# Performance work log

Hardware: AMD Instinct MI355X
Metric: run time of the kernel (lower is better)

Reference implementation:

```python
import jax, jax.numpy as jnp
import numpy as np

NUM_CLASSES = 80
STRIDES = (8, 16, 32)
RADIUS = 2.5
BOX_WEIGHT = 5.0
BIG = 1e9  # emulates restriction of cost/matching to union-candidate anchors
CAND_K = 10


def setup_inputs() -> dict:
    key = jax.random.key(0)
    ks = jax.random.split(key, 6)
    B, G = 16, 16
    p0 = jax.random.normal(ks[0], (B, NUM_CLASSES + 5, 160, 160), jnp.float32)
    p1 = jax.random.normal(ks[1], (B, NUM_CLASSES + 5, 80, 80), jnp.float32)
    p2 = jax.random.normal(ks[2], (B, NUM_CLASSES + 5, 40, 40), jnp.float32)
    cxy = jax.random.uniform(ks[3], (B, G, 2), jnp.float32, 64.0, 1216.0)
    wh = jax.random.uniform(ks[4], (B, G, 2), jnp.float32, 16.0, 256.0)
    cls = jax.random.randint(ks[5], (B, G, 1), 0, NUM_CLASSES).astype(jnp.float32)
    labels = jnp.concatenate([cxy, wh, cls], axis=-1)  # [B,G,5] xywh + class id
    return {"p0": p0, "p1": p1, "p2": p2, "labels": labels}


def _decode(p, stride):
    # [B,C,H,W] -> [B,HW,C] with xy=(xy+grid)*stride, wh=exp(wh)*stride
    B, C, H, W = p.shape
    out = jnp.transpose(p.reshape(B, C, H * W), (0, 2, 1))
    yy, xx = jnp.meshgrid(jnp.arange(H, dtype=p.dtype), jnp.arange(W, dtype=p.dtype), indexing='ij')
    gx, gy = xx.reshape(-1), yy.reshape(-1)
    xy = (out[..., :2] + jnp.stack([gx, gy], axis=-1)) * stride
    wh = jnp.exp(out[..., 2:4]) * stride
    return jnp.concatenate([xy, wh, out[..., 4:]], axis=-1), gx, gy


def _pair_iou(a, b):
    # a:[G,4], b:[A,4] in xywh -> [G,A]
    a1, a2 = a[:, :2] - a[:, 2:] * 0.5, a[:, :2] + a[:, 2:] * 0.5
    b1, b2 = b[:, :2] - b[:, 2:] * 0.5, b[:, :2] + b[:, 2:] * 0.5
    tl = jnp.maximum(a1[:, None], b1[None])
    br = jnp.minimum(a2[:, None], b2[None])
    wh = jnp.maximum(br - tl, 0.0)
    inter = wh[..., 0] * wh[..., 1]
    return inter / (a[:, 2] * a[:, 3])[:, None].__add__((b[:, 2] * b[:, 3])[None]).__sub__(inter).__add__(1e-16)


def _elem_iou(a, b):
    # elementwise xywh iou on [...,4]
    a1, a2 = a[..., :2] - a[..., 2:] * 0.5, a[..., :2] + a[..., 2:] * 0.5
    b1, b2 = b[..., :2] - b[..., 2:] * 0.5, b[..., :2] + b[..., 2:] * 0.5
    wh = jnp.maximum(jnp.minimum(a2, b2) - jnp.maximum(a1, b1), 0.0)
    inter = wh[..., 0] * wh[..., 1]
    return inter / (a[..., 2] * a[..., 3] + b[..., 2] * b[..., 3] - inter + 1e-16)


def _bce_logits(x, t):
    return jnp.maximum(x, 0.0) - x * t + jnp.log1p(jnp.exp(-jnp.abs(x)))


def _assign(tb, tc, pbox, pcls_l, pconf_l, xc, yc, sv):
    # Per-image SimOTA. tb:[G,4] tc:[G] pbox:[A,4] pcls_l:[A,C] pconf_l:[A]
    G = tb.shape[0]
    bx, by, bw, bh = tb[:, 0:1], tb[:, 1:2], tb[:, 2:3], tb[:, 3:4]
    in_box = (xc[None] > bx - bw * 0.5) & (xc[None] < bx + bw * 0.5) & \
             (yc[None] > by - bh * 0.5) & (yc[None] < by + bh * 0.5)  # [G,A]
    r = RADIUS * sv[None]
    in_mir = (xc[None] > bx - r) & (xc[None] < bx + r) & (yc[None] > by - r) & (yc[None] < by + r)
    union = jnp.any(in_box, 0) | jnp.any(in_mir, 0)  # [A]
    inter = in_box & in_mir  # [G,A]
    iou = _pair_iou(tb, pbox)  # [G,A]
    # cls cost: BCE(sqrt(sigmoid(cls)*sigmoid(conf)), one_hot) summed over classes
    p = jnp.sqrt(jax.nn.sigmoid(pcls_l) * jax.nn.sigmoid(pconf_l)[:, None])  # [A,C]
    logp = jnp.clip(jnp.log(p), -100.0, None)
    log1mp = jnp.clip(jnp.log1p(-p), -100.0, None)
    base = -log1mp.sum(-1)  # [A] = sum_c -log(1-p)
    cls_cost = base[None] - logp[:, tc].T + log1mp[:, tc].T  # [G,A]
    cost = cls_cost - 3.0 * jnp.log(iou + 1e-8) + 1e5 * (~inter) + BIG * (~union)[None]
    iou_m = jnp.where(union[None], iou, 0.0)
    dyn_k = jnp.maximum(jax.lax.top_k(iou_m, CAND_K)[0].sum(1).astype(jnp.int32), 1)  # [G]
    _, idx = jax.lax.top_k(-cost, CAND_K)  # per-gt lowest-cost anchors, sorted
    sel = (jnp.arange(CAND_K)[None] < dyn_k[:, None]).astype(cost.dtype)  # [G,K]
    matching = jnp.zeros_like(cost).at[jnp.arange(G)[:, None], idx].max(sel)  # [G,A]
    conflict = matching.sum(0) > 1.0
    gt_min = jnp.argmin(cost, axis=0)  # [A]
    onehot_min = (jnp.arange(G)[:, None] == gt_min[None]).astype(cost.dtype)
    matching = jnp.where(conflict[None], onehot_min, matching)
    fg = matching.sum(0) > 0.0  # [A]
    gidx = jnp.argmax(matching, axis=0)  # [A]
    miou = (matching * iou).sum(0)  # [A]
    t_cls = jax.nn.one_hot(tc[gidx], NUM_CLASSES, dtype=cost.dtype) * miou[:, None]  # [A,C]
    t_box = tb[gidx]  # [A,4]
    return fg, t_cls, t_box


def _forward(p0, p1, p2, labels):
    outs, xcs, ycs, svs = [], [], [], []
    for p, s in zip((p0, p1, p2), STRIDES):
        o, gx, gy = _decode(p, float(s))
        outs.append(o)
        xcs.append((gx + 0.5) * s)
        ycs.append((gy + 0.5) * s)
        svs.append(jnp.full_like(gx, s))
    out = jnp.concatenate(outs, axis=1)  # [B,A,85]
    xc, yc, sv = jnp.concatenate(xcs), jnp.concatenate(ycs), jnp.concatenate(svs)
    pbox, pconf, pcls = out[..., :4], out[..., 4], out[..., 5:]
    tb, tc = labels[..., :4], labels[..., 4].astype(jnp.int32)
    assign = jax.vmap(_assign, in_axes=(0, 0, 0, 0, 0, None, None, None))
    fg, t_cls, t_box = jax.lax.stop_gradient(assign(tb, tc, pbox, pcls, pconf, xc, yc, sv))
    fgf = fg.astype(pbox.dtype)  # target_conf == final fg mask
    loss_box = (fgf * (1.0 - _elem_iou(pbox, t_box) ** 2)).sum()
    loss_conf = _bce_logits(pconf, fgf).sum()
    loss_cls = (fgf[..., None] * _bce_logits(pcls, t_cls)).sum()
    fg_num = jnp.maximum(fgf.sum(), 1.0)
    return (BOX_WEIGHT * loss_box + loss_conf + loss_cls) / fg_num


def reference(p0, p1, p2, labels):
    return _forward(p0, p1, p2, labels)
```

## Files before the change

### kernel.cpp

```cpp
#include <hip/hip_runtime.h>
#include <hip/hip_bf16.h>
#include <cstdint>

#define NCLS 80
#define GNUM 16
#define BNUM 16
#define A0   25600
#define A1   6400
#define A2   1600
#define ATOT 33600
#define QTOT 16800
#define NBLK_A 132
#define NBLK_TOTAL (NBLK_A*BNUM)
#define NSPLIT 8
#define SEG   4200
#define WSEG  1050
#define NWAVE 32
#define FINF  3.4e38f
#define IINF  0x7fffffff

__device__ __forceinline__ float rcpf(float x){ return __builtin_amdgcn_rcpf(x); }
__device__ __forceinline__ float sqf (float x){ return __builtin_amdgcn_sqrtf(x); }
__device__ __forceinline__ float rsqf(float x){ return __builtin_amdgcn_rsqf(x); }

__device__ __forceinline__ float bce(float x, float t){
  float e = __expf(-fabsf(x));
  return fmaxf(x,0.f) - x*t + __logf(1.f + e);
}

__device__ __forceinline__ void get_level(const float* p0, const float* p1, const float* p2,
                                          int a, const float*& p, int& hw, int& off, int& W, float& s)
{
  if (a < A0){ p=p0; hw=A0; off=a; W=160; s=8.f; }
  else if (a < A0+A1){ p=p1; hw=A1; off=a-A0; W=80; s=16.f; }
  else { p=p2; hw=A2; off=a-A0-A1; W=40; s=32.f; }
}

__global__ __launch_bounds__(256, 4) void decode_cost_kernel(
    const float* __restrict__ p0, const float* __restrict__ p1, const float* __restrict__ p2,
    const float* __restrict__ labels,
    float* __restrict__ cost, float4* __restrict__ pbox, float* __restrict__ pconf,
    unsigned char* __restrict__ unionm)
{
  const int b = blockIdx.y;
  const int q = blockIdx.x*256 + threadIdx.x;
  __shared__ float s_tb[GNUM][4];
  __shared__ int   s_tc[GNUM];
  if (threadIdx.x < GNUM){
    const float* L = labels + ((size_t)b*GNUM + threadIdx.x)*5;
    s_tb[threadIdx.x][0]=L[0]; s_tb[threadIdx.x][1]=L[1];
    s_tb[threadIdx.x][2]=L[2]; s_tb[threadIdx.x][3]=L[3];
    s_tc[threadIdx.x]=(int)L[4];
  }
  __syncthreads();
  if (q >= QTOT) return;
  const int a0 = q*2;

  const float* p; int hw, off, W; float s;
  get_level(p0,p1,p2,a0,p,hw,off,W,s);
  const float* bp = p + (size_t)b*(NCLS+5)*hw + off;

  const float2 RX = *(const float2*)(bp);
  const float2 RY = *(const float2*)(bp + (size_t)hw);
  const float2 RW = *(const float2*)(bp + 2*(size_t)hw);
  const float2 RH = *(const float2*)(bp + 3*(size_t)hw);
  const float2 CL = *(const float2*)(bp + 4*(size_t)hw);
  const float* cp = bp + 5*(size_t)hw;

  int gx0 = off % W, gy0 = off / W;
  int gx1 = gx0+1, gy1 = gy0; if (gx1 >= W){ gx1 = 0; gy1++; }

  const float sc0 = rcpf(1.f + __expf(-CL.x));
  const float sc1 = rcpf(1.f + __expf(-CL.y));
  const float ssc0 = sqf(sc0),   ssc1 = sqf(sc1);
  const float rssc0 = rcpf(ssc0), rssc1 = rcpf(ssc1);

  float base0=0.f, base1=0.f;
  #pragma unroll 2
  for (int bt=0; bt<10; bt++){
    float2 xv[8];
    #pragma unroll
    for (int j=0;j<8;j++) xv[j] = *(const float2*)(cp + (size_t)(bt*8+j)*hw);
    float pr0=1.f, pr1=1.f;
    #pragma unroll
    for (int j=0;j<8;j++){
      pr0 *= (1.f - ssc0*rsqf(1.f+__expf(-xv[j].x)));
      pr1 *= (1.f - ssc1*rsqf(1.f+__expf(-xv[j].y)));
    }
    base0 -= __logf(pr0);
    base1 -= __logf(pr1);
  }

  const float px0=(RX.x+gx0)*s, py0=(RY.x+gy0)*s, pw0=__expf(RW.x)*s, ph0=__expf(RH.x)*s;
  const float px1=(RX.y+gx1)*s, py1=(RY.y+gy1)*s, pw1=__expf(RW.y)*s, ph1=__expf(RH.y)*s;
  const float xc0=(gx0+0.5f)*s, yc0=(gy0+0.5f)*s;
  const float xc1=(gx1+0.5f)*s, yc1=(gy1+0.5f)*s;
  const float q1x0=px0-pw0*0.5f, q2x0=px0+pw0*0.5f, q1y0=py0-ph0*0.5f, q2y0=py0+ph0*0.5f;
  const float q1x1=px1-pw1*0.5f, q2x1=px1+pw1*0.5f, q1y1=py1-ph1*0.5f, q2y1=py1+ph1*0.5f;
  const float areaP0 = pw0*ph0, areaP1 = pw1*ph1;
  const float r = 2.5f*s;

  bool un0=false, un1=false;
  #pragma unroll
  for (int g=0;g<GNUM;g++){
    const float bx=s_tb[g][0], by=s_tb[g][1], bw=s_tb[g][2], bh=s_tb[g][3];
    const float b1x=bx-bw*0.5f, b2x=bx+bw*0.5f, b1y=by-bh*0.5f, b2y=by+bh*0.5f;
    un0 = un0 || ((xc0>b1x)&&(xc0<b2x)&&(yc0>b1y)&&(yc0<b2y))
              || ((xc0>bx-r)&&(xc0<bx+r)&&(yc0>by-r)&&(yc0<by+r));
    un1 = un1 || ((xc1>b1x)&&(xc1<b2x)&&(yc1>b1y)&&(yc1<b2y))
              || ((xc1>bx-r)&&(xc1<bx+r)&&(yc1>by-r)&&(yc1<by+r));
  }
  const float add0 = un0?0.f:1e9f, add1 = un1?0.f:1e9f;

  const size_t rowb = (size_t)b*GNUM*ATOT + a0;

  #pragma unroll
  for (int g=0;g<GNUM;g++){
    const float2 x = *(const float2*)(cp + (size_t)s_tc[g]*hw);
    const float e0 = __expf(-x.x), e1 = __expf(-x.y);
    const float rp0 = rssc0*sqf(1.f+e0), rp1 = rssc1*sqf(1.f+e1);
    const float cd0 = __logf(fmaxf(rp0-1.f, 1e-30f));
    const float cd1 = __logf(fmaxf(rp1-1.f, 1e-30f));

    const float bx=s_tb[g][0], by=s_tb[g][1], bw=s_tb[g][2], bh=s_tb[g][3];
    const float b1x=bx-bw*0.5f, b2x=bx+bw*0.5f, b1y=by-bh*0.5f, b2y=by+bh*0.5f;
    const float areaB = bw*bh;

    const bool inb0 = (xc0>b1x)&&(xc0<b2x)&&(yc0>b1y)&&(yc0<b2y);
    const bool inm0 = (xc0>bx-r)&&(xc0<bx+r)&&(yc0>by-r)&&(yc0<by+r);
    const bool inb1 = (xc1>b1x)&&(xc1<b2x)&&(yc1>b1y)&&(yc1<b2y);
    const bool inm1 = (xc1>bx-r)&&(xc1<bx+r)&&(yc1>by-r)&&(yc1<by+r);

    float iw,ih,inte;
    iw = fmaxf(fminf(b2x,q2x0)-fmaxf(b1x,q1x0),0.f);
    ih = fmaxf(fminf(b2y,q2y0)-fmaxf(b1y,q1y0),0.f);
    inte = iw*ih;
    const float iou0 = inte * rcpf(areaB+areaP0-inte+1e-16f);
    iw = fmaxf(fminf(b2x,q2x1)-fmaxf(b1x,q1x1),0.f);
    ih = fmaxf(fminf(b2y,q2y1)-fmaxf(b1y,q1y1),0.f);
    inte = iw*ih;
    const float iou1 = inte * rcpf(areaB+areaP1-inte+1e-16f);

    float2 cst;
    cst.x = base0 + cd0 - 3.f*__logf(iou0+1e-8f) + ((inb0&&inm0)?0.f:100000.f) + add0;
    cst.y = base1 + cd1 - 3.f*__logf(iou1+1e-8f) + ((inb1&&inm1)?0.f:100000.f) + add1;
    *(float2*)(cost + rowb + (size_t)g*ATOT) = cst;
  }

  pbox[(size_t)b*ATOT+a0  ] = make_float4(px0,py0,pw0,ph0);
  pbox[(size_t)b*ATOT+a0+1] = make_float4(px1,py1,pw1,ph1);
  *(float2*)(pconf + (size_t)b*ATOT + a0) = make_float2(CL.x, CL.y);
  uchar2 um; um.x = un0?1:0; um.y = un1?1:0;
  *(uchar2*)(unionm + (size_t)b*ATOT + a0) = um;
}

__global__ __launch_bounds__(256) void topk_stage1(
    const float* __restrict__ cost, const float4* __restrict__ pbox,
    const unsigned char* __restrict__ unionm, const float* __restrict__ labels,
    float* __restrict__ cand_c, int* __restrict__ cand_i, float* __restrict__ cand_v)
{
  const int bg   = blockIdx.y;
  const int b    = bg >> 4;
  const int seg  = blockIdx.x;
  const int wave = threadIdx.x >> 6;
  const int lane = threadIdx.x & 63;
  const int wg   = seg*4 + wave;

  const float*  crow = cost + (size_t)bg*ATOT;
  const float4* prow = pbox + (size_t)b*ATOT;
  const unsigned char* urow = unionm + (size_t)b*ATOT;
  const float bx = labels[bg*5+0], by = labels[bg*5+1];
  const float bw = labels[bg*5+2], bh = labels[bg*5+3];
  const float areaB = bw*bh;
  const float b1x=bx-bw*0.5f, b2x=bx+bw*0.5f, b1y=by-bh*0.5f, b2y=by+bh*0.5f;

  const int start = seg*SEG + wave*WSEG;
  const int end   = start + WSEG;

  float cv[10]; int ci[10]; float iv[10];
  #pragma unroll
  for (int k=0;k<10;k++){ cv[k]=FINF; ci[k]=IINF; iv[k]=0.f; }

  for (int a = start + lane; a < end; a += 64){
    float c = crow[a];
    if (c < cv[9] || (c == cv[9] && a < ci[9])){
      float nc=c; int ni=a;
      #pragma unroll
      for (int k=0;k<10;k++){
        bool better = (nc < cv[k]) || (nc==cv[k] && ni<ci[k]);
        float tv=cv[k]; int ti=ci[k];
        cv[k]=better?nc:cv[k]; ci[k]=better?ni:ci[k];
        nc  =better?tv:nc;     ni  =better?ti:ni;
      }
    }
    if (urow[a]){
      float4 pb = prow[a];
      float tlx=fmaxf(b1x, pb.x-pb.z*0.5f), brx=fminf(b2x, pb.x+pb.z*0.5f);
      float tly=fmaxf(b1y, pb.y-pb.w*0.5f), bry=fminf(b2y, pb.y+pb.w*0.5f);
      float iw=fmaxf(brx-tlx,0.f), ih=fmaxf(bry-tly,0.f);
      float inte=iw*ih;
      float io = inte * rcpf(areaB + pb.z*pb.w - inte + 1e-16f);
      if (io > iv[9]){
        float nv=io;
        #pragma unroll
        for (int k=0;k<10;k++){
          bool better = nv > iv[k];
          float tv=iv[k];
          iv[k]=better?nv:iv[k];
          nv  =better?tv:nv;
        }
      }
    }
  }

  float selc = 0.f; int seli = 0;
  #pragma unroll
  for (int r=0;r<10;r++){
    float bv = cv[0]; int bi = ci[0];
    #pragma unroll
    for (int off=32; off>0; off>>=1){
      float ov = __shfl_xor(bv, off);
      int   oi = __shfl_xor(bi, off);
      bool take = (ov < bv) || (ov==bv && oi<bi);
      bv = take?ov:bv; bi = take?oi:bi;
    }
    if (lane == r){ selc = bv; seli = bi; }
    if (cv[0]==bv && ci[0]==bi){
      #pragma unroll
      for (int k=0;k<9;k++){ cv[k]=cv[k+1]; ci[k]=ci[k+1]; }
      cv[9]=FINF; ci[9]=IINF;
    }
  }
  float selv = 0.f;
  #pragma unroll
  for (int r=0;r<10;r++){
    float bv = iv[0]; int bl = lane;
    #pragma unroll
    for (int off=32; off>0; off>>=1){
      float ov = __shfl_xor(bv, off);
      int   ol = __shfl_xor(bl, off);
      bool take = (ov > bv) || (ov==bv && ol<bl);
      bv = take?ov:bv; bl = take?ol:bl;
    }
    if (lane == r) selv = bv;
    if (lane == bl){
      #pragma unroll
      for (int k=0;k<9;k++){ iv[k]=iv[k+1]; }
      iv[9]=0.f;
    }
  }

  if (lane < 10){
    const size_t base = ((size_t)bg*NWAVE + wg)*10 + lane;
    cand_c[base] = selc;
    cand_i[base] = seli;
    cand_v[base] = selv;
  }
}

__global__ __launch_bounds__(64) void topk_stage2(
    const float* __restrict__ cand_c, const int* __restrict__ cand_i,
    const float* __restrict__ cand_v, unsigned int* __restrict__ match_mask)
{
  const int bg = blockIdx.x;
  const int b = bg >> 4, g = bg & 15;
  const int lane = threadIdx.x;
  const size_t base = (size_t)bg*NWAVE*10 + lane*5;

  float cv[5]; int ci[5]; float iv[5];
  #pragma unroll
  for (int k=0;k<5;k++){ cv[k]=cand_c[base+k]; ci[k]=cand_i[base+k]; iv[k]=cand_v[base+k]; }

  int seli = 0;
  #pragma unroll
  for (int r=0;r<10;r++){
    float bv = cv[0]; int bi = ci[0];
    #pragma unroll
    for (int off=32; off>0; off>>=1){
      float ov = __shfl_xor(bv, off);
      int   oi = __shfl_xor(bi, off);
      bool take = (ov < bv) || (ov==bv && oi<bi);
      bv = take?ov:bv; bi = take?oi:bi;
    }
    if (lane == r) seli = bi;
    if (cv[0]==bv && ci[0]==bi){
      #pragma unroll
      for (int k=0;k<4;k++){ cv[k]=cv[k+1]; ci[k]=ci[k+1]; }
      cv[4]=FINF; ci[4]=IINF;
    }
  }

  float isum = 0.f;
  #pragma unroll
  for (int r=0;r<10;r++){
    float bv = iv[0]; int bl = lane;
    #pragma unroll
    for (int off=32; off>0; off>>=1){
      float ov = __shfl_xor(bv, off);
      int   ol = __shfl_xor(bl, off);
      bool take = (ov > bv) || (ov==bv && ol<bl);
      bv = take?ov:bv; bl = take?ol:bl;
    }
    isum += bv;
    if (lane == bl){
      #pragma unroll
      for (int k=0;k<4;k++){ iv[k]=iv[k+1]; }
      iv[4]=0.f;
    }
  }

  int dynk = (int)isum;
  if (dynk < 1)  dynk = 1;
  if (dynk > 10) dynk = 10;
  if (lane < dynk)
    atomicOr(&match_mask[(size_t)b*ATOT + seli], 1u<<g);
}

__global__ __launch_bounds__(256) void loss_kernel(
    const float* __restrict__ p0, const float* __restrict__ p1, const float* __restrict__ p2,
    const float* __restrict__ labels,
    const float* __restrict__ cost, const float4* __restrict__ pbox,
    const float* __restrict__ pconf, const unsigned int* __restrict__ match_mask,
    float* __restrict__ blocksums)
{
  const int b = blockIdx.y;
  const int a = blockIdx.x*256 + threadIdx.x;
  float lbox=0.f, lconf=0.f, lcls=0.f, fgn=0.f;
  if (a < ATOT){
    unsigned int m = match_mask[(size_t)b*ATOT+a];
    float cl = pconf[(size_t)b*ATOT+a];
    if (m != 0u){
      int gidx;
      if (__popc(m) > 1){
        float best = FINF; int bgi = 0;
        for (int g=0; g<GNUM; g++){
          float c = cost[((size_t)b*GNUM+g)*ATOT + a];
          if (c < best){ best=c; bgi=g; }
        }
        gidx = bgi;
      } else {
        gidx = __ffs(m)-1;
      }
      const float* L = labels + ((size_t)b*GNUM+gidx)*5;
      float bx=L[0], by=L[1], bw=L[2], bh=L[3];
      int tcg=(int)L[4];
      float4 pb = pbox[(size_t)b*ATOT+a];
      float tlx=fmaxf(bx-bw*0.5f, pb.x-pb.z*0.5f);
      float brx=fminf(bx+bw*0.5f, pb.x+pb.z*0.5f);
      float tly=fmaxf(by-bh*0.5f, pb.y-pb.w*0.5f);
      float bry=fminf(by+bh*0.5f, pb.y+pb.w*0.5f);
      float iw=fmaxf(brx-tlx,0.f), ih=fmaxf(bry-tly,0.f);
      float inte=iw*ih;
      float iou = inte * rcpf(bw*bh + pb.z*pb.w - inte + 1e-16f);
      lbox = 1.f - iou*iou;
      lconf = bce(cl, 1.f);
      float miou = iou;
      const float* p; int hw, off, W; float s;
      get_level(p0,p1,p2,a,p,hw,off,W,s);
      const float* bp = p + (size_t)b*(NCLS+5)*hw + off;
      for (int c=0;c<NCLS;c++){
        float x = bp[(size_t)(5+c)*hw];
        float t = (c==tcg)? miou : 0.f;
        lcls += bce(x, t);
      }
      fgn = 1.f;
    } else {
      lconf = bce(cl, 0.f);
    }
  }
  #pragma unroll
  for (int off2=32; off2>0; off2>>=1){
    lbox  += __shfl_down(lbox,  off2);
    lconf += __shfl_down(lconf, off2);
    lcls  += __shfl_down(lcls,  off2);
    fgn   += __shfl_down(fgn,   off2);
  }
  __shared__ float s_red[4][4];
  const int wave = threadIdx.x >> 6;
  if ((threadIdx.x & 63)==0){
    s_red[wave][0]=lbox; s_red[wave][1]=lconf; s_red[wave][2]=lcls; s_red[wave][3]=fgn;
  }
  __syncthreads();
  if (threadIdx.x==0){
    float r0=0,r1=0,r2=0,r3=0;
    #pragma unroll
    for (int w=0;w<4;w++){ r0+=s_red[w][0]; r1+=s_red[w][1]; r2+=s_red[w][2]; r3+=s_red[w][3]; }
    const int bid = blockIdx.y*gridDim.x + blockIdx.x;
    ((float4*)blocksums)[bid] = make_float4(r0,r1,r2,r3);
  }
}

__global__ __launch_bounds__(256) void finalize_kernel(
    const float* __restrict__ blocksums, float* __restrict__ out)
{
  const int tid = threadIdx.x;
  float r0=0,r1=0,r2=0,r3=0;
  for (int i = tid; i < NBLK_TOTAL; i += 256){
    const float4 v = ((const float4*)blocksums)[i];
    r0+=v.x; r1+=v.y; r2+=v.z; r3+=v.w;
  }
  #pragma unroll
  for (int off=32; off>0; off>>=1){
    r0 += __shfl_down(r0, off);
    r1 += __shfl_down(r1, off);
    r2 += __shfl_down(r2, off);
    r3 += __shfl_down(r3, off);
  }
  __shared__ float s_red[4][4];
  const int wave = tid >> 6;
  if ((tid & 63)==0){ s_red[wave][0]=r0; s_red[wave][1]=r1; s_red[wave][2]=r2; s_red[wave][3]=r3; }
  __syncthreads();
  if (tid==0){
    float t0=0,t1=0,t2=0,t3=0;
    #pragma unroll
    for (int w=0;w<4;w++){ t0+=s_red[w][0]; t1+=s_red[w][1]; t2+=s_red[w][2]; t3+=s_red[w][3]; }
    out[0] = (5.f*t0 + t1 + t2) / fmaxf(t3, 1.f);
  }
}

extern "C" void kernel_launch(void* const* d_in, const int* in_sizes, int n_in,
                              void* d_out, int out_size, void* d_ws, size_t ws_size,
                              hipStream_t stream)
{
  const float* p0     = (const float*)d_in[0];
  const float* p1     = (const float*)d_in[1];
  const float* p2     = (const float*)d_in[2];
  const float* labels = (const float*)d_in[3];

  char* ws = (char*)d_ws;
  size_t o = 0;
  float*        cost       = (float*)(ws + o);        o += (size_t)BNUM*GNUM*ATOT*4;
  float4*       pbox       = (float4*)(ws + o);       o += (size_t)BNUM*ATOT*16;
  float*        pconf      = (float*)(ws + o);        o += (size_t)BNUM*ATOT*4;
  unsigned int* match_mask = (unsigned int*)(ws + o); o += (size_t)BNUM*ATOT*4;
  unsigned char* unionm    = (unsigned char*)(ws + o);o += (size_t)BNUM*ATOT;
  o = (o + 255) & ~(size_t)255;
  float*        blocksums  = (float*)(ws + o);        o += (size_t)NBLK_TOTAL*4*4;
  o = (o + 255) & ~(size_t)255;
  float*        cand_c     = (float*)(ws + o);        o += (size_t)256*NWAVE*10*4;
  int*          cand_i     = (int*)(ws + o);          o += (size_t)256*NWAVE*10*4;
  float*        cand_v     = (float*)(ws + o);        o += (size_t)256*NWAVE*10*4;

  hipMemsetAsync(match_mask, 0, (size_t)BNUM*ATOT*4, stream);

  dim3 gridA((QTOT+255)/256, BNUM);
  decode_cost_kernel<<<gridA, 256, 0, stream>>>(p0,p1,p2,labels,cost,pbox,pconf,unionm);
  dim3 gridT(NSPLIT, BNUM*GNUM);
  topk_stage1<<<gridT, 256, 0, stream>>>(cost, pbox, unionm, labels, cand_c, cand_i, cand_v);
  topk_stage2<<<BNUM*GNUM, 64, 0, stream>>>(cand_c, cand_i, cand_v, match_mask);
  dim3 gridC(NBLK_A, BNUM);
  loss_kernel<<<gridC, 256, 0, stream>>>(p0,p1,p2,labels,cost,pbox,pconf,match_mask,blocksums);
  finalize_kernel<<<1, 256, 0, stream>>>(blocksums, (float*)d_out);
}
```

Measured before the change: 142.9 us.

## Split decode-cost work across four lanes per anchor pair with shuffle reductions

Each anchor pair is now handled by four threads. Each thread computes a quarter of the class-product base cost (20 classes), a quarter of the union tests (4 GT boxes) and a quarter of the cost rows. Partial results are combined with xor shuffles, and only lane 0 writes the per-anchor outputs. The goal is more threads and waves in the decode/cost kernel, with fewer registers per thread, to hide memory latency better. The cost is some redundant box and decode arithmetic per lane, more blocks, and less coalesced stores, since adjacent lanes now write to different cost rows.

Result: no change. 142.7 us (-0.2%).

```diff
diff --git a/kernel.cpp b/kernel.cpp
--- a/kernel.cpp
+++ b/kernel.cpp
@@ -36,36 +36,37 @@
   else { p=p2; hw=A2; off=a-A0-A1; W=40; s=32.f; }
 }
 
-__global__ __launch_bounds__(256, 4) void decode_cost_kernel(
+__global__ __launch_bounds__(256, 8) void decode_cost_kernel(
     const float* __restrict__ p0, const float* __restrict__ p1, const float* __restrict__ p2,
     const float* __restrict__ labels,
     float* __restrict__ cost, float4* __restrict__ pbox, float* __restrict__ pconf,
     unsigned char* __restrict__ unionm)
 {
   const int b = blockIdx.y;
-  const int q = blockIdx.x*256 + threadIdx.x;
+  const int t = threadIdx.x;
   __shared__ float s_tb[GNUM][4];
   __shared__ int   s_tc[GNUM];
-  if (threadIdx.x < GNUM){
-    const float* L = labels + ((size_t)b*GNUM + threadIdx.x)*5;
-    s_tb[threadIdx.x][0]=L[0]; s_tb[threadIdx.x][1]=L[1];
-    s_tb[threadIdx.x][2]=L[2]; s_tb[threadIdx.x][3]=L[3];
-    s_tc[threadIdx.x]=(int)L[4];
+  if (t < GNUM){
+    const float* L = labels + ((size_t)b*GNUM + t)*5;
+    s_tb[t][0]=L[0]; s_tb[t][1]=L[1]; s_tb[t][2]=L[2]; s_tb[t][3]=L[3];
+    s_tc[t]=(int)L[4];
   }
   __syncthreads();
+  const int q = blockIdx.x*64 + (t>>2);
+  const int k = t & 3;
   if (q >= QTOT) return;
   const int a0 = q*2;
 
   const float* p; int hw, off, W; float s;
   get_level(p0,p1,p2,a0,p,hw,off,W,s);
   const float* bp = p + (size_t)b*(NCLS+5)*hw + off;
+  const float* cp = bp + 5*(size_t)hw;
 
   const float2 RX = *(const float2*)(bp);
   const float2 RY = *(const float2*)(bp + (size_t)hw);
   const float2 RW = *(const float2*)(bp + 2*(size_t)hw);
   const float2 RH = *(const float2*)(bp + 3*(size_t)hw);
   const float2 CL = *(const float2*)(bp + 4*(size_t)hw);
-  const float* cp = bp + 5*(size_t)hw;
 
   int gx0 = off % W, gy0 = off / W;
   int gx1 = gx0+1, gy1 = gy0; if (gx1 >= W){ gx1 = 0; gy1++; }
@@ -75,21 +76,46 @@
   const float ssc0 = sqf(sc0),   ssc1 = sqf(sc1);
   const float rssc0 = rcpf(ssc0), rssc1 = rcpf(ssc1);
 
-  float base0=0.f, base1=0.f;
-  #pragma unroll 2
-  for (int bt=0; bt<10; bt++){
+  float part0 = 0.f, part1 = 0.f;
+  const int cb = 20*k;
+  {
     float2 xv[8];
     #pragma unroll
-    for (int j=0;j<8;j++) xv[j] = *(const float2*)(cp + (size_t)(bt*8+j)*hw);
+    for (int j=0;j<8;j++) xv[j] = *(const float2*)(cp + (size_t)(cb+j)*hw);
     float pr0=1.f, pr1=1.f;
     #pragma unroll
     for (int j=0;j<8;j++){
       pr0 *= (1.f - ssc0*rsqf(1.f+__expf(-xv[j].x)));
       pr1 *= (1.f - ssc1*rsqf(1.f+__expf(-xv[j].y)));
     }
-    base0 -= __logf(pr0);
-    base1 -= __logf(pr1);
-  }
+    part0 -= __logf(pr0); part1 -= __logf(pr1);
+  }
+  {
+    float2 xv[8];
+    #pragma unroll
+    for (int j=0;j<8;j++) xv[j] = *(const float2*)(cp + (size_t)(cb+8+j)*hw);
+    float pr0=1.f, pr1=1.f;
+    #pragma unroll
+    for (int j=0;j<8;j++){
+      pr0 *= (1.f - ssc0*rsqf(1.f+__expf(-xv[j].x)));
+      pr1 *= (1.f - ssc1*rsqf(1.f+__expf(-xv[j].y)));
+    }
+    part0 -= __logf(pr0); part1 -= __logf(pr1);
+  }
+  {
+    float2 xv[4];
+    #pragma unroll
+    for (int j=0;j<4;j++) xv[j] = *(const float2*)(cp + (size_t)(cb+16+j)*hw);
+    float pr0=1.f, pr1=1.f;
+    #pragma unroll
+    for (int j=0;j<4;j++){
+      pr0 *= (1.f - ssc0*rsqf(1.f+__expf(-xv[j].x)));
+      pr1 *= (1.f - ssc1*rsqf(1.f+__expf(-xv[j].y)));
+    }
+    part0 -= __logf(pr0); part1 -= __logf(pr1);
+  }
+  float base0 = part0 + __shfl_xor(part0, 1); base0 += __shfl_xor(base0, 2);
+  float base1 = part1 + __shfl_xor(part1, 1); base1 += __shfl_xor(base1, 2);
 
   const float px0=(RX.x+gx0)*s, py0=(RY.x+gy0)*s, pw0=__expf(RW.x)*s, ph0=__expf(RH.x)*s;
   const float px1=(RX.y+gx1)*s, py1=(RY.y+gy1)*s, pw1=__expf(RW.y)*s, ph1=__expf(RH.y)*s;
@@ -100,22 +126,27 @@
   const float areaP0 = pw0*ph0, areaP1 = pw1*ph1;
   const float r = 2.5f*s;
 
-  bool un0=false, un1=false;
-  #pragma unroll
-  for (int g=0;g<GNUM;g++){
+  int mybits = 0;
+  #pragma unroll
+  for (int j=0;j<4;j++){
+    const int g = k*4 + j;
     const float bx=s_tb[g][0], by=s_tb[g][1], bw=s_tb[g][2], bh=s_tb[g][3];
     const float b1x=bx-bw*0.5f, b2x=bx+bw*0.5f, b1y=by-bh*0.5f, b2y=by+bh*0.5f;
-    un0 = un0 || ((xc0>b1x)&&(xc0<b2x)&&(yc0>b1y)&&(yc0<b2y))
-              || ((xc0>bx-r)&&(xc0<bx+r)&&(yc0>by-r)&&(yc0<by+r));
-    un1 = un1 || ((xc1>b1x)&&(xc1<b2x)&&(yc1>b1y)&&(yc1<b2y))
-              || ((xc1>bx-r)&&(xc1<bx+r)&&(yc1>by-r)&&(yc1<by+r));
-  }
-  const float add0 = un0?0.f:1e9f, add1 = un1?0.f:1e9f;
+    const bool u0 = ((xc0>b1x)&&(xc0<b2x)&&(yc0>b1y)&&(yc0<b2y))
+                  || ((xc0>bx-r)&&(xc0<bx+r)&&(yc0>by-r)&&(yc0<by+r));
+    const bool u1 = ((xc1>b1x)&&(xc1<b2x)&&(yc1>b1y)&&(yc1<b2y))
+                  || ((xc1>bx-r)&&(xc1<bx+r)&&(yc1>by-r)&&(yc1<by+r));
+    mybits |= (u0?1:0) | (u1?2:0);
+  }
+  mybits |= __shfl_xor(mybits, 1);
+  mybits |= __shfl_xor(mybits, 2);
+  const float add0 = (mybits&1)?0.f:1e9f, add1 = (mybits&2)?0.f:1e9f;
 
   const size_t rowb = (size_t)b*GNUM*ATOT + a0;
 
   #pragma unroll
-  for (int g=0;g<GNUM;g++){
+  for (int j=0;j<4;j++){
+    const int g = k*4 + j;
     const float2 x = *(const float2*)(cp + (size_t)s_tc[g]*hw);
     const float e0 = __expf(-x.x), e1 = __expf(-x.y);
     const float rp0 = rssc0*sqf(1.f+e0), rp1 = rssc1*sqf(1.f+e1);
@@ -147,11 +178,13 @@
     *(float2*)(cost + rowb + (size_t)g*ATOT) = cst;
   }
 
-  pbox[(size_t)b*ATOT+a0  ] = make_float4(px0,py0,pw0,ph0);
-  pbox[(size_t)b*ATOT+a0+1] = make_float4(px1,py1,pw1,ph1);
-  *(float2*)(pconf + (size_t)b*ATOT + a0) = make_float2(CL.x, CL.y);
-  uchar2 um; um.x = un0?1:0; um.y = un1?1:0;
-  *(uchar2*)(unionm + (size_t)b*ATOT + a0) = um;
+  if (k == 0){
+    pbox[(size_t)b*ATOT+a0  ] = make_float4(px0,py0,pw0,ph0);
+    pbox[(size_t)b*ATOT+a0+1] = make_float4(px1,py1,pw1,ph1);
+    *(float2*)(pconf + (size_t)b*ATOT + a0) = make_float2(CL.x, CL.y);
+    uchar2 um; um.x = (mybits&1)?1:0; um.y = (mybits&2)?1:0;
+    *(uchar2*)(unionm + (size_t)b*ATOT + a0) = um;
+  }
 }
 
 __global__ __launch_bounds__(256) void topk_stage1(
@@ -443,7 +476,7 @@
 
   hipMemsetAsync(match_mask, 0, (size_t)BNUM*ATOT*4, stream);
 
-  dim3 gridA((QTOT+255)/256, BNUM);
+  dim3 gridA((QTOT + 63)/64, BNUM);
   decode_cost_kernel<<<gridA, 256, 0, stream>>>(p0,p1,p2,labels,cost,pbox,pconf,unionm);
   dim3 gridT(NSPLIT, BNUM*GNUM);
   topk_stage1<<<gridT, 256, 0, stream>>>(cost, pbox, unionm, labels, cand_c, cand_i, cand_v);
```
